# Kernel optimization log

Hardware: AMD Instinct MI355X
Metric: run time of the kernel (lower is better)

The kernel has to match this reference:

```python
import jax, jax.numpy as jnp
import numpy as np

NEG_SLOPE = 0.2

def gat_conv(x, src, dst, W, a_src, a_dst, b, n_nodes):
    # x: [N, Fin] -> h: [N, Fout]; edges (src->dst) incl. self-loops
    h = x @ W                                   # [N, Fout]
    as_ = h @ a_src                             # [N] per-node source score
    ad_ = h @ a_dst                             # [N] per-node dest score
    e = jax.nn.leaky_relu(as_[src] + ad_[dst], NEG_SLOPE)   # [E]
    # segment softmax over edges sharing the same destination
    e_max = jax.ops.segment_max(e, dst, num_segments=n_nodes)
    e_exp = jnp.exp(e - e_max[dst])
    e_sum = jax.ops.segment_sum(e_exp, dst, num_segments=n_nodes)
    alpha = e_exp / (e_sum[dst] + 1e-16)        # [E]
    out = jax.ops.segment_sum(alpha[:, None] * h[src], dst, num_segments=n_nodes)
    return out + b

def setup_inputs() -> dict:
    key = jax.random.key(0)
    ks = jax.random.split(key, 12)
    N, E, Fin, H = 100000, 3200000, 128, 32
    def g(k, shape, scale):
        return jax.random.normal(k, shape, dtype=jnp.float32) * scale
    return {
        "x": g(ks[0], (N, Fin), 1.0),
        "edge_index": jax.random.randint(ks[1], (2, E), 0, N, dtype=jnp.int32),
        "W1": g(ks[2], (Fin, H), 1.0 / np.sqrt(Fin)),
        "att_src1": g(ks[3], (H,), 1.0 / np.sqrt(H)),
        "att_dst1": g(ks[4], (H,), 1.0 / np.sqrt(H)),
        "b1": jnp.zeros((H,), jnp.float32),
        "W2": g(ks[5], (H, H), 1.0 / np.sqrt(H)),
        "att_src2": g(ks[6], (H,), 1.0 / np.sqrt(H)),
        "att_dst2": g(ks[7], (H,), 1.0 / np.sqrt(H)),
        "b2": jnp.zeros((H,), jnp.float32),
        "Wf": g(ks[8], (H, H), 1.0 / np.sqrt(H)),
        "bf": jnp.zeros((H,), jnp.float32),
    }

def reference(x, edge_index, W1, att_src1, att_dst1, b1, W2, att_src2, att_dst2, b2, Wf, bf):
    n_nodes = x.shape[0]
    loops = jnp.arange(n_nodes, dtype=edge_index.dtype)
    src = jnp.concatenate([edge_index[0], loops])  # add_self_loops=True (PyG default)
    dst = jnp.concatenate([edge_index[1], loops])
    h = jax.nn.relu(gat_conv(x, src, dst, W1, att_src1, att_dst1, b1, n_nodes))
    h = jax.nn.relu(gat_conv(h, src, dst, W2, att_src2, att_dst2, b2, n_nodes))
    return h @ Wf + bf
```

## Files before the change

### kernel.cpp

```cpp
#include <hip/hip_runtime.h>

#define NEG_SLOPE 0.2f
#define BK_SH 8
#define BK_SZ 256
#define MAXBUCK 512
#define EPB 8192

typedef _Float16 half8 __attribute__((ext_vector_type(8)));
typedef float f32x4 __attribute__((ext_vector_type(4)));

__global__ __launch_bounds__(256) void k_castW(const float* __restrict__ W,
                                               _Float16* __restrict__ Wt,
                                               int K) {
  for (int i = threadIdx.x; i < K * 32; i += 256) {
    int k = i >> 5, f = i & 31;
    Wt[f * K + k] = (_Float16)W[i];
  }
}

__global__ __launch_bounds__(256) void k_feat1(
    const float* __restrict__ x, const _Float16* __restrict__ Wt,
    const float* __restrict__ a_src, const float* __restrict__ a_dst,
    _Float16* __restrict__ Hh, float* __restrict__ as_, float* __restrict__ ad_,
    int N) {
  int w = threadIdx.x >> 6;
  int lane = threadIdx.x & 63;
  int base = (blockIdx.x * 4 + w) * 16;
  if (base >= N) return;
  int row16 = lane & 15;
  int kg = lane >> 4;
  f32x4 acc0 = {0.f, 0.f, 0.f, 0.f};
  f32x4 acc1 = {0.f, 0.f, 0.f, 0.f};
  const float* xr = x + (size_t)(base + row16) * 128 + kg * 8;
#pragma unroll
  for (int kt = 0; kt < 4; ++kt) {
    float4 u0 = *reinterpret_cast<const float4*>(xr + kt * 32);
    float4 u1 = *reinterpret_cast<const float4*>(xr + kt * 32 + 4);
    half8 a;
    a[0] = (_Float16)u0.x; a[1] = (_Float16)u0.y;
    a[2] = (_Float16)u0.z; a[3] = (_Float16)u0.w;
    a[4] = (_Float16)u1.x; a[5] = (_Float16)u1.y;
    a[6] = (_Float16)u1.z; a[7] = (_Float16)u1.w;
    half8 b0 = *reinterpret_cast<const half8*>(Wt + (size_t)row16 * 128 +
                                               kt * 32 + kg * 8);
    half8 b1 = *reinterpret_cast<const half8*>(Wt + (size_t)(16 + row16) * 128 +
                                               kt * 32 + kg * 8);
    acc0 = __builtin_amdgcn_mfma_f32_16x16x32_f16(a, b0, acc0, 0, 0, 0);
    acc1 = __builtin_amdgcn_mfma_f32_16x16x32_f16(a, b1, acc1, 0, 0, 0);
  }
  float aS0 = a_src[row16], aS1 = a_src[16 + row16];
  float aD0 = a_dst[row16], aD1 = a_dst[16 + row16];
  float tS[4], tD[4];
#pragma unroll
  for (int r = 0; r < 4; ++r) {
    int row = base + kg * 4 + r;
    Hh[(size_t)row * 32 + row16] = (_Float16)acc0[r];
    Hh[(size_t)row * 32 + 16 + row16] = (_Float16)acc1[r];
    tS[r] = acc0[r] * aS0 + acc1[r] * aS1;
    tD[r] = acc0[r] * aD0 + acc1[r] * aD1;
  }
#pragma unroll
  for (int off = 1; off <= 8; off <<= 1) {
#pragma unroll
    for (int r = 0; r < 4; ++r) {
      tS[r] += __shfl_xor(tS[r], off, 64);
      tD[r] += __shfl_xor(tD[r], off, 64);
    }
  }
  if (row16 == 0) {
#pragma unroll
    for (int r = 0; r < 4; ++r) {
      as_[base + kg * 4 + r] = tS[r];
      ad_[base + kg * 4 + r] = tD[r];
    }
  }
}

__global__ __launch_bounds__(256) void k_feat2(
    const _Float16* __restrict__ Bh, const _Float16* __restrict__ Wt,
    const float* __restrict__ a_src, const float* __restrict__ a_dst,
    _Float16* __restrict__ Hh, float* __restrict__ as_, float* __restrict__ ad_,
    int N) {
  int w = threadIdx.x >> 6;
  int lane = threadIdx.x & 63;
  int base = (blockIdx.x * 4 + w) * 16;
  if (base >= N) return;
  int row16 = lane & 15;
  int kg = lane >> 4;
  half8 a = *reinterpret_cast<const half8*>(Bh + (size_t)(base + row16) * 32 +
                                            kg * 8);
  half8 b0 =
      *reinterpret_cast<const half8*>(Wt + (size_t)row16 * 32 + kg * 8);
  half8 b1 =
      *reinterpret_cast<const half8*>(Wt + (size_t)(16 + row16) * 32 + kg * 8);
  f32x4 acc0 = {0.f, 0.f, 0.f, 0.f};
  f32x4 acc1 = {0.f, 0.f, 0.f, 0.f};
  acc0 = __builtin_amdgcn_mfma_f32_16x16x32_f16(a, b0, acc0, 0, 0, 0);
  acc1 = __builtin_amdgcn_mfma_f32_16x16x32_f16(a, b1, acc1, 0, 0, 0);
  float aS0 = a_src[row16], aS1 = a_src[16 + row16];
  float aD0 = a_dst[row16], aD1 = a_dst[16 + row16];
  float tS[4], tD[4];
#pragma unroll
  for (int r = 0; r < 4; ++r) {
    int row = base + kg * 4 + r;
    Hh[(size_t)row * 32 + row16] = (_Float16)acc0[r];
    Hh[(size_t)row * 32 + 16 + row16] = (_Float16)acc1[r];
    tS[r] = acc0[r] * aS0 + acc1[r] * aS1;
    tD[r] = acc0[r] * aD0 + acc1[r] * aD1;
  }
#pragma unroll
  for (int off = 1; off <= 8; off <<= 1) {
#pragma unroll
    for (int r = 0; r < 4; ++r) {
      tS[r] += __shfl_xor(tS[r], off, 64);
      tD[r] += __shfl_xor(tD[r], off, 64);
    }
  }
  if (row16 == 0) {
#pragma unroll
    for (int r = 0; r < 4; ++r) {
      as_[base + kg * 4 + r] = tS[r];
      ad_[base + kg * 4 + r] = tD[r];
    }
  }
}

__global__ __launch_bounds__(256) void k_zero(int* __restrict__ p, int n) {
  int i = blockIdx.x * 256 + threadIdx.x;
  if (i < n) p[i] = 0;
}

__global__ __launch_bounds__(256) void k_bhist(const int* __restrict__ ei,
                                               int E, int* __restrict__ bcnt,
                                               int nbuck) {
  __shared__ int h[MAXBUCK];
  for (int i = threadIdx.x; i < nbuck; i += 256) h[i] = 0;
  __syncthreads();
  long base = (long)blockIdx.x * EPB;
#pragma unroll 4
  for (int i = 0; i < EPB / 256; ++i) {
    long e = base + i * 256 + threadIdx.x;
    if (e < E) atomicAdd(&h[ei[E + e] >> BK_SH], 1);
  }
  __syncthreads();
  for (int i = threadIdx.x; i < nbuck; i += 256)
    if (h[i]) atomicAdd(&bcnt[i], h[i]);
}

__global__ __launch_bounds__(1024) void k_scan(const int* __restrict__ bcnt,
                                               int* __restrict__ boff,
                                               int* __restrict__ bcur,
                                               int* __restrict__ ptr, int nbuck,
                                               int N, int E) {
  __shared__ int s[1024];
  int t = threadIdx.x;
  int v = (t < nbuck) ? bcnt[t] : 0;
  s[t] = v;
  __syncthreads();
  for (int off = 1; off < 1024; off <<= 1) {
    int x = (t >= off) ? s[t - off] : 0;
    __syncthreads();
    s[t] += x;
    __syncthreads();
  }
  if (t < nbuck) {
    boff[t] = s[t] - v;
    bcur[t] = s[t] - v;
  }
  if (t == 0) {
    boff[nbuck] = E;
    ptr[N] = E;
  }
}

__global__ __launch_bounds__(256) void k_binA(const int* __restrict__ ei, int E,
                                              int* __restrict__ bcur,
                                              unsigned* __restrict__ packed,
                                              int nbuck) {
  __shared__ int h[MAXBUCK];
  __shared__ int lbase[MAXBUCK];
  __shared__ int lb[MAXBUCK];
  __shared__ int cur[MAXBUCK];
  __shared__ int psum[256];
  __shared__ unsigned rec[EPB];
  __shared__ unsigned short bkt[EPB];
  int t = threadIdx.x;
  for (int i = t; i < MAXBUCK; i += 256) h[i] = 0;
  __syncthreads();
  long base = (long)blockIdx.x * EPB;
  int cnt = (int)((E - base) < EPB ? (E - base) : EPB);
#pragma unroll 4
  for (int i = 0; i < EPB / 256; ++i) {
    int e = i * 256 + t;
    if (e < cnt) atomicAdd(&h[ei[E + base + e] >> BK_SH], 1);
  }
  __syncthreads();
  for (int i = t; i < nbuck; i += 256)
    lbase[i] = h[i] ? atomicAdd(&bcur[i], h[i]) : 0;
  int a0 = h[2 * t], a1 = h[2 * t + 1];
  psum[t] = a0 + a1;
  __syncthreads();
  for (int off = 1; off < 256; off <<= 1) {
    int x = (t >= off) ? psum[t - off] : 0;
    __syncthreads();
    psum[t] += x;
    __syncthreads();
  }
  int pex = psum[t] - (a0 + a1);
  lb[2 * t] = pex;
  lb[2 * t + 1] = pex + a0;
  cur[2 * t] = pex;
  cur[2 * t + 1] = pex + a0;
  __syncthreads();
#pragma unroll 4
  for (int i = 0; i < EPB / 256; ++i) {
    int e = i * 256 + t;
    if (e < cnt) {
      int s = ei[base + e], d = ei[E + base + e];
      int b = d >> BK_SH;
      int pos = atomicAdd(&cur[b], 1);
      rec[pos] = ((unsigned)s << 8) | (unsigned)(d & (BK_SZ - 1));
      bkt[pos] = (unsigned short)b;
    }
  }
  __syncthreads();
  for (int i = t; i < cnt; i += 256) {
    int b = bkt[i];
    packed[(size_t)lbase[b] + (i - lb[b])] = rec[i];
  }
}

__global__ __launch_bounds__(256) void k_binB(const unsigned* __restrict__ packed,
                                              const int* __restrict__ boff,
                                              int* __restrict__ ptr,
                                              int* __restrict__ srcs, int N) {
  int b = blockIdx.x;
  int beg = boff[b], end = boff[b + 1];
  int t = threadIdx.x;
  __shared__ int lcnt[BK_SZ];
  __shared__ int sc[BK_SZ];
  __shared__ int lcur[BK_SZ];
  lcnt[t] = 0;
  __syncthreads();
  for (int i = beg + t; i < end; i += 256)
    atomicAdd(&lcnt[packed[i] & (BK_SZ - 1)], 1);
  __syncthreads();
  int v = lcnt[t];
  sc[t] = v;
  __syncthreads();
  for (int off = 1; off < 256; off <<= 1) {
    int x = (t >= off) ? sc[t - off] : 0;
    __syncthreads();
    sc[t] += x;
    __syncthreads();
  }
  int excl = sc[t] - v;
  int node = (b << BK_SH) + t;
  if (node < N) ptr[node] = beg + excl;
  lcur[t] = excl;
  __syncthreads();
  for (int i = beg + t; i < end; i += 256) {
    unsigned p = packed[i];
    int slot = atomicAdd(&lcur[p & (BK_SZ - 1)], 1);
    srcs[(size_t)beg + slot] = (int)(p >> 8);
  }
}

template <int FINAL>
__global__ __launch_bounds__(256) void k_gatherT(
    const int* __restrict__ ptr, const int* __restrict__ srcs,
    const _Float16* __restrict__ Hh, const float* __restrict__ as_,
    const float* __restrict__ ad_, const float* __restrict__ b,
    const float* __restrict__ Wf, const float* __restrict__ bf,
    void* __restrict__ OUTv, int N) {
  __shared__ float sWf[32 * 32];
  __shared__ float sO[8][33];
  if (FINAL) {
    for (int i = threadIdx.x; i < 32 * 32; i += 256) sWf[i] = Wf[i];
  }
  int g = threadIdx.x >> 5;
  int lane = threadIdx.x & 31;
  int sub = lane >> 2;
  int q = lane & 3;
  int d = blockIdx.x * 8 + g;
  int dc = d < N ? d : N - 1;
  float ad_d = ad_[dc];
  float acc[8] = {0.f, 0.f, 0.f, 0.f, 0.f, 0.f, 0.f, 0.f};
  float sumw = 0.f;
  int beg = ptr[dc], end = ptr[dc + 1];
  bool v0 = sub < end - beg;
  int sid0 = v0 ? srcs[beg + sub] : dc;
  float sa0 = as_[sid0];
  half8 hv0 = *reinterpret_cast<const half8*>(Hh + (size_t)sid0 * 32 + q * 8);
  bool v1 = sub < end - (beg + 8);
  int sid1 = v1 ? srcs[beg + 8 + sub] : dc;
  float sa1 = as_[sid1];
  half8 hv1 = *reinterpret_cast<const half8*>(Hh + (size_t)sid1 * 32 + q * 8);
  for (int j = beg; j < end; j += 8) {
    int jn = j + 16;
    bool v2 = sub < end - jn;
    int sid2 = v2 ? srcs[jn + sub] : dc;
    float sa2 = as_[sid2];
    half8 hv2 = *reinterpret_cast<const half8*>(Hh + (size_t)sid2 * 32 + q * 8);
    float sc2 = sa0 + ad_d;
    float el = sc2 > 0.f ? sc2 : NEG_SLOPE * sc2;
    float w = v0 ? __expf(el) : 0.f;
#pragma unroll
    for (int i = 0; i < 8; ++i) acc[i] += w * (float)hv0[i];
    sumw += w;
    v0 = v1; sid0 = sid1; sa0 = sa1; hv0 = hv1;
    v1 = v2; sid1 = sid2; sa1 = sa2; hv1 = hv2;
  }
#pragma unroll
  for (int off = 4; off <= 16; off <<= 1) {
#pragma unroll
    for (int i = 0; i < 8; ++i) acc[i] += __shfl_xor(acc[i], off, 32);
    sumw += __shfl_xor(sumw, off, 32);
  }
  if (sub == 0) {
    float s0 = as_[dc] + ad_d;
    float e0 = s0 > 0.f ? s0 : NEG_SLOPE * s0;
    float w0 = __expf(e0);
    half8 hs = *reinterpret_cast<const half8*>(Hh + (size_t)dc * 32 + q * 8);
#pragma unroll
    for (int i = 0; i < 8; ++i) acc[i] += w0 * (float)hs[i];
    sumw += w0;
    float inv = 1.f / (sumw + 1e-16f);
    if (FINAL) {
#pragma unroll
      for (int i = 0; i < 8; ++i)
        sO[g][q * 8 + i] = fmaxf(acc[i] * inv + b[q * 8 + i], 0.f);
    } else if (d < N) {
      half8 o;
#pragma unroll
      for (int i = 0; i < 8; ++i)
        o[i] = (_Float16)fmaxf(acc[i] * inv + b[q * 8 + i], 0.f);
      *reinterpret_cast<half8*>((_Float16*)OUTv + (size_t)d * 32 + q * 8) = o;
    }
  }
  if (FINAL) {
    __syncthreads();
    float accf = bf[lane];
#pragma unroll
    for (int k = 0; k < 32; ++k) accf += sO[g][k] * sWf[k * 32 + lane];
    if (d < N) ((float*)OUTv)[(size_t)d * 32 + lane] = accf;
  }
}

extern "C" void kernel_launch(void* const* d_in, const int* in_sizes, int n_in,
                              void* d_out, int out_size, void* d_ws,
                              size_t ws_size, hipStream_t stream) {
  const float* x = (const float*)d_in[0];
  const int* ei = (const int*)d_in[1];
  const float* W1 = (const float*)d_in[2];
  const float* as1 = (const float*)d_in[3];
  const float* ad1 = (const float*)d_in[4];
  const float* b1 = (const float*)d_in[5];
  const float* W2 = (const float*)d_in[6];
  const float* as2 = (const float*)d_in[7];
  const float* ad2 = (const float*)d_in[8];
  const float* b2 = (const float*)d_in[9];
  const float* Wf = (const float*)d_in[10];
  const float* bf = (const float*)d_in[11];
  float* out = (float*)d_out;

  const int H = in_sizes[3];
  const int FIN = in_sizes[2] / H;
  const int N = in_sizes[0] / FIN;
  const int E = in_sizes[1] / 2;
  const int nbuck = (N + BK_SZ - 1) >> BK_SH;
  (void)n_in; (void)out_size; (void)ws_size; (void)H;

  size_t r0 = (size_t)E * 4;
  size_t bhB = (size_t)N * 32 * 2;
  if (bhB > r0) r0 = bhB;
  char* basep = (char*)d_ws;
  unsigned* packed = (unsigned*)basep;
  _Float16* Bh = (_Float16*)basep;
  char* p = basep + r0;
  _Float16* Hh = (_Float16*)p;   p += (size_t)N * 32 * 2;
  _Float16* Wt1 = (_Float16*)p;  p += (size_t)128 * 32 * 2;
  _Float16* Wt2 = (_Float16*)p;  p += (size_t)32 * 32 * 2;
  float* asv = (float*)p;        p += (size_t)N * 4;
  float* adv = (float*)p;        p += (size_t)N * 4;
  int* ptr = (int*)p;            p += (size_t)(N + 1) * 4;
  int* srcs = (int*)p;           p += (size_t)E * 4;
  int* bcnt = (int*)p;           p += (size_t)nbuck * 4;
  int* boff = (int*)p;           p += (size_t)(nbuck + 1) * 4;
  int* bcur = (int*)p;

  const int nodeBlocks = (N + 7) / 8;
  const int binBlocks = (E + EPB - 1) / EPB;
  const int mfmaBlocks = (N / 16 + 3) / 4;

  k_zero<<<(nbuck + 255) / 256, 256, 0, stream>>>(bcnt, nbuck);
  k_bhist<<<binBlocks, 256, 0, stream>>>(ei, E, bcnt, nbuck);
  k_scan<<<1, 1024, 0, stream>>>(bcnt, boff, bcur, ptr, nbuck, N, E);
  k_binA<<<binBlocks, 256, 0, stream>>>(ei, E, bcur, packed, nbuck);
  k_binB<<<nbuck, 256, 0, stream>>>(packed, boff, ptr, srcs, N);

  k_castW<<<1, 256, 0, stream>>>(W1, Wt1, 128);
  k_castW<<<1, 256, 0, stream>>>(W2, Wt2, 32);

  k_feat1<<<mfmaBlocks, 256, 0, stream>>>(x, Wt1, as1, ad1, Hh, asv, adv, N);
  k_gatherT<0><<<nodeBlocks, 256, 0, stream>>>(ptr, srcs, Hh, asv, adv, b1,
                                               nullptr, nullptr, Bh, N);

  k_feat2<<<mfmaBlocks, 256, 0, stream>>>(Bh, Wt2, as2, ad2, Hh, asv, adv, N);
  k_gatherT<1><<<nodeBlocks, 256, 0, stream>>>(ptr, srcs, Hh, asv, adv, b2, Wf,
                                               bf, out, N);
}
```

Before: 220.2 us.

## Store per-block bucket histograms and scan them instead of recounting in binning

```diff
diff --git a/kernel.cpp b/kernel.cpp
--- a/kernel.cpp
+++ b/kernel.cpp
@@ -132,6 +132,7 @@
 
 __global__ __launch_bounds__(256) void k_bhist(const int* __restrict__ ei,
                                                int E, int* __restrict__ bcnt,
+                                               int* __restrict__ hmat,
                                                int nbuck) {
   __shared__ int h[MAXBUCK];
   for (int i = threadIdx.x; i < nbuck; i += 256) h[i] = 0;
@@ -143,13 +144,15 @@
     if (e < E) atomicAdd(&h[ei[E + e] >> BK_SH], 1);
   }
   __syncthreads();
-  for (int i = threadIdx.x; i < nbuck; i += 256)
+  int* hrow = hmat + (size_t)blockIdx.x * nbuck;
+  for (int i = threadIdx.x; i < nbuck; i += 256) {
+    hrow[i] = h[i];
     if (h[i]) atomicAdd(&bcnt[i], h[i]);
+  }
 }
 
 __global__ __launch_bounds__(1024) void k_scan(const int* __restrict__ bcnt,
                                                int* __restrict__ boff,
-                                               int* __restrict__ bcur,
                                                int* __restrict__ ptr, int nbuck,
                                                int N, int E) {
   __shared__ int s[1024];
@@ -163,40 +166,48 @@
     s[t] += x;
     __syncthreads();
   }
-  if (t < nbuck) {
-    boff[t] = s[t] - v;
-    bcur[t] = s[t] - v;
-  }
+  if (t < nbuck) boff[t] = s[t] - v;
   if (t == 0) {
     boff[nbuck] = E;
     ptr[N] = E;
   }
 }
 
-__global__ __launch_bounds__(256) void k_binA(const int* __restrict__ ei, int E,
-                                              int* __restrict__ bcur,
-                                              unsigned* __restrict__ packed,
-                                              int nbuck) {
+__global__ __launch_bounds__(512) void k_colscan(const int* __restrict__ hmat,
+                                                 int* __restrict__ lbg,
+                                                 const int* __restrict__ boff,
+                                                 int nb, int nbuck) {
+  int t = threadIdx.x;
+  if (t >= nbuck) return;
+  int base = boff[t];
+  for (int blk = 0; blk < nb; ++blk) {
+    size_t idx = (size_t)blk * nbuck + t;
+    int v = hmat[idx];
+    lbg[idx] = base;
+    base += v;
+  }
+}
+
+__global__ __launch_bounds__(256) void k_binA(
+    const int* __restrict__ ei, int E, const int* __restrict__ hmat,
+    const int* __restrict__ lbg, unsigned* __restrict__ packed, int nbuck) {
   __shared__ int h[MAXBUCK];
   __shared__ int lbase[MAXBUCK];
   __shared__ int lb[MAXBUCK];
   __shared__ int cur[MAXBUCK];
   __shared__ int psum[256];
   __shared__ unsigned rec[EPB];
-  __shared__ unsigned short bkt[EPB];
+  __shared__ unsigned char bkt[EPB];
   int t = threadIdx.x;
-  for (int i = t; i < MAXBUCK; i += 256) h[i] = 0;
+  const int* hrow = hmat + (size_t)blockIdx.x * nbuck;
+  const int* brow = lbg + (size_t)blockIdx.x * nbuck;
+  for (int i = t; i < MAXBUCK; i += 256) {
+    h[i] = (i < nbuck) ? hrow[i] : 0;
+    lbase[i] = (i < nbuck) ? brow[i] : 0;
+  }
   __syncthreads();
   long base = (long)blockIdx.x * EPB;
   int cnt = (int)((E - base) < EPB ? (E - base) : EPB);
-#pragma unroll 4
-  for (int i = 0; i < EPB / 256; ++i) {
-    int e = i * 256 + t;
-    if (e < cnt) atomicAdd(&h[ei[E + base + e] >> BK_SH], 1);
-  }
-  __syncthreads();
-  for (int i = t; i < nbuck; i += 256)
-    lbase[i] = h[i] ? atomicAdd(&bcur[i], h[i]) : 0;
   int a0 = h[2 * t], a1 = h[2 * t + 1];
   psum[t] = a0 + a1;
   __syncthreads();
@@ -220,12 +231,13 @@
       int b = d >> BK_SH;
       int pos = atomicAdd(&cur[b], 1);
       rec[pos] = ((unsigned)s << 8) | (unsigned)(d & (BK_SZ - 1));
-      bkt[pos] = (unsigned short)b;
+      bkt[pos] = (unsigned char)b;
     }
   }
   __syncthreads();
   for (int i = t; i < cnt; i += 256) {
-    int b = bkt[i];
+    int b0 = bkt[i];
+    int b = (i >= lb[b0] && i < cur[b0]) ? b0 : b0 + 256;
     packed[(size_t)lbase[b] + (i - lb[b])] = rec[i];
   }
 }
@@ -296,7 +308,10 @@
   int sid1 = v1 ? srcs[beg + 8 + sub] : dc;
   float sa1 = as_[sid1];
   half8 hv1 = *reinterpret_cast<const half8*>(Hh + (size_t)sid1 * 32 + q * 8);
-  for (int j = beg; j < end; j += 8) {
+  int nb8 = (end - beg + 7) >> 3;
+  int j = beg;
+#pragma unroll 2
+  for (int it = 0; it < nb8; ++it) {
     int jn = j + 16;
     bool v2 = sub < end - jn;
     int sid2 = v2 ? srcs[jn + sub] : dc;
@@ -308,6 +323,7 @@
 #pragma unroll
     for (int i = 0; i < 8; ++i) acc[i] += w * (float)hv0[i];
     sumw += w;
+    j = j + 8;
     v0 = v1; sid0 = sid1; sa0 = sa1; hv0 = hv1;
     v1 = v2; sid1 = sid2; sa1 = sa2; hv1 = hv2;
   }
@@ -371,6 +387,10 @@
   const int nbuck = (N + BK_SZ - 1) >> BK_SH;
   (void)n_in; (void)out_size; (void)ws_size; (void)H;
 
+  const int nodeBlocks = (N + 7) / 8;
+  const int binBlocks = (E + EPB - 1) / EPB;
+  const int mfmaBlocks = (N / 16 + 3) / 4;
+
   size_t r0 = (size_t)E * 4;
   size_t bhB = (size_t)N * 32 * 2;
   if (bhB > r0) r0 = bhB;
@@ -387,16 +407,14 @@
   int* srcs = (int*)p;           p += (size_t)E * 4;
   int* bcnt = (int*)p;           p += (size_t)nbuck * 4;
   int* boff = (int*)p;           p += (size_t)(nbuck + 1) * 4;
-  int* bcur = (int*)p;
-
-  const int nodeBlocks = (N + 7) / 8;
-  const int binBlocks = (E + EPB - 1) / EPB;
-  const int mfmaBlocks = (N / 16 + 3) / 4;
+  int* hmat = (int*)p;           p += (size_t)binBlocks * nbuck * 4;
+  int* lbg = (int*)p;
 
   k_zero<<<(nbuck + 255) / 256, 256, 0, stream>>>(bcnt, nbuck);
-  k_bhist<<<binBlocks, 256, 0, stream>>>(ei, E, bcnt, nbuck);
-  k_scan<<<1, 1024, 0, stream>>>(bcnt, boff, bcur, ptr, nbuck, N, E);
-  k_binA<<<binBlocks, 256, 0, stream>>>(ei, E, bcur, packed, nbuck);
+  k_bhist<<<binBlocks, 256, 0, stream>>>(ei, E, bcnt, hmat, nbuck);
+  k_scan<<<1, 1024, 0, stream>>>(bcnt, boff, ptr, nbuck, N, E);
+  k_colscan<<<1, 512, 0, stream>>>(hmat, lbg, boff, binBlocks, nbuck);
+  k_binA<<<binBlocks, 256, 0, stream>>>(ei, E, hmat, lbg, packed, nbuck);
   k_binB<<<nbuck, 256, 0, stream>>>(packed, boff, ptr, srcs, N);
 
   k_castW<<<1, 256, 0, stream>>>(W1, Wt1, 128);
```

Result: slower. 305.4 us (+38.7%).
